# Kernel optimization log

Hardware: AMD Instinct MI355X
Metric: run time of the kernel (lower is better)

## Reference

```python
import jax, jax.numpy as jnp
import numpy as np

B_, J_, D_, E_, N_, K_ = 32, 1024, 192, 384, 16, 3


def _dwconv(x, w, b):
    # x: (B,J,E), w: (E,1,K) depthwise, b: (E,)
    xc = jnp.transpose(x, (0, 2, 1))  # (B,E,J)
    pad = w.shape[2] // 2
    y = jax.lax.conv_general_dilated(
        xc, w, window_strides=(1,), padding=[(pad, pad)],
        feature_group_count=w.shape[0], dimension_numbers=('NCH', 'OIH', 'NCH'))
    return jnp.transpose(y + b[None, :, None], (0, 2, 1))  # (B,J,E)


def _scan_dir(x, cw, cb, WB, bB, WC, bC, WD, bD, A, Wi, bi, Wr, br):
    # One directional selective-SSM pass. x: (B,J,E); A: (N,) negative diag.
    xc = _dwconv(x, cw, cb)                       # (B,J,E)
    Bt = xc @ WB + bB                             # (B,J,N)
    Ct = xc @ WC + bC                             # (B,J,N)
    Dt = jax.nn.softplus(xc @ WD + bD)            # Delta, (B,J,N)
    A_bar = jnp.exp(Dt * A)                       # ZOH discretization
    B_bar = (A_bar - 1.0) / (A + 1e-6) * Bt
    u = xc @ Wi + bi                              # in_to_state, (B,J,N)
    Bu = B_bar * u

    def step(h, ab_bu):
        ab, bu = ab_bu
        h = ab * h + bu
        return h, h

    h0 = jnp.zeros((x.shape[0], A.shape[0]), x.dtype)
    _, hs = jax.lax.scan(step, h0, (jnp.swapaxes(A_bar, 0, 1), jnp.swapaxes(Bu, 0, 1)))
    hs = jnp.swapaxes(hs, 0, 1)                   # (B,J,N)
    return (hs * Ct) @ Wr + br                    # readout, (B,J,E)


def setup_inputs() -> dict:
    key = jax.random.key(0)
    ks = iter(jax.random.split(key, 40))

    def nrm(shape, scale=0.02):
        return jax.random.normal(next(ks), shape, jnp.float32) * scale

    inp = {
        'tokens': jax.random.normal(next(ks), (B_, J_, D_), jnp.float32),
        'norm_g': jnp.ones((D_,), jnp.float32),
        'norm_b': jnp.zeros((D_,), jnp.float32),
        'Wx': nrm((D_, E_)), 'bx': jnp.zeros((E_,), jnp.float32),
        'Wz': nrm((D_, E_)), 'bz': jnp.zeros((E_,), jnp.float32),
        'convf_w': nrm((E_, 1, K_), 0.1), 'convf_b': jnp.zeros((E_,), jnp.float32),
        'convb_w': nrm((E_, 1, K_), 0.1), 'convb_b': jnp.zeros((E_,), jnp.float32),
        'WBf': nrm((E_, N_)), 'bBf': jnp.zeros((N_,), jnp.float32),
        'WCf': nrm((E_, N_)), 'bCf': jnp.zeros((N_,), jnp.float32),
        'WDf': nrm((E_, N_)), 'bDf': jnp.zeros((N_,), jnp.float32),
        'WBb': nrm((E_, N_)), 'bBb': jnp.zeros((N_,), jnp.float32),
        'WCb': nrm((E_, N_)), 'bCb': jnp.zeros((N_,), jnp.float32),
        'WDb': nrm((E_, N_)), 'bDb': jnp.zeros((N_,), jnp.float32),
        'A_log': nrm((N_,), 0.5),
        'Wi': nrm((E_, N_)), 'bi': jnp.zeros((N_,), jnp.float32),
        'Wr': nrm((N_, E_)), 'br': jnp.zeros((E_,), jnp.float32),
        'Wo': nrm((E_, D_)), 'bo': jnp.zeros((D_,), jnp.float32),
    }
    return inp


def reference(tokens, norm_g, norm_b, Wx, bx, Wz, bz, convf_w, convf_b,
              convb_w, convb_b, WBf, bBf, WCf, bCf, WDf, bDf, WBb, bBb,
              WCb, bCb, WDb, bDb, A_log, Wi, bi, Wr, br, Wo, bo):
    # LayerNorm (biased variance, eps=1e-5, like torch)
    mu = jnp.mean(tokens, axis=-1, keepdims=True)
    var = jnp.mean(jnp.square(tokens - mu), axis=-1, keepdims=True)
    t = (tokens - mu) / jnp.sqrt(var + 1e-5) * norm_g + norm_b

    x = t @ Wx + bx
    z = t @ Wz + bz
    gate = jax.nn.sigmoid(jax.nn.silu(z))

    # A computed under no_grad in torch -> stop_gradient here
    A = jax.lax.stop_gradient(-jax.nn.softplus(A_log))

    y_f = _scan_dir(x, convf_w, convf_b, WBf, bBf, WCf, bCf, WDf, bDf, A, Wi, bi, Wr, br)
    y_b = jnp.flip(_scan_dir(jnp.flip(x, 1), convb_w, convb_b, WBb, bBb, WCb, bCb,
                             WDb, bDb, A, Wi, bi, Wr, br), 1)
    y = (y_f + y_b) * gate
    return tokens + y @ Wo + bo
```

## Files before the change

### kernel.cpp

```cpp
#include <hip/hip_runtime.h>
#include <math.h>


typedef __attribute__((ext_vector_type(8))) short short8;
typedef __attribute__((ext_vector_type(4))) float f32x4;

__device__ __forceinline__ unsigned short f2bf(float f){
  union { float f; unsigned u; } v; v.f = f;
  unsigned r = v.u + 0x7FFFu + ((v.u >> 16) & 1u);
  return (unsigned short)(r >> 16);
}
__device__ __forceinline__ float bf2f(unsigned short s){
  union { unsigned u; float f; } v; v.u = ((unsigned)s) << 16;
  return v.f;
}
__device__ __forceinline__ float softplusf(float x){
  return (x > 20.f) ? x : log1pf(expf(x));
}
__device__ __forceinline__ float sigf(float x){
  return 1.f / (1.f + expf(-x));
}

__global__ __launch_bounds__(256) void prep_kernel(
    const float* __restrict__ Wx, const float* __restrict__ Wz,
    const float* __restrict__ WBf, const float* __restrict__ WCf,
    const float* __restrict__ WDf, const float* __restrict__ WBb,
    const float* __restrict__ WCb, const float* __restrict__ WDb,
    const float* __restrict__ Wi, const float* __restrict__ Wr,
    const float* __restrict__ Wo,
    const float* __restrict__ bBf, const float* __restrict__ bCf,
    const float* __restrict__ bDf, const float* __restrict__ bBb,
    const float* __restrict__ bCb, const float* __restrict__ bDb,
    const float* __restrict__ bi,
    unsigned short* __restrict__ Wxz_t, unsigned short* __restrict__ W4f_t,
    unsigned short* __restrict__ W4b_t, unsigned short* __restrict__ Wrt2,
    unsigned short* __restrict__ Wot, float* __restrict__ b4f,
    float* __restrict__ b4b)
{
  int idx = blockIdx.x * 256 + threadIdx.x;
  if (idx < 147456){ int n = idx / 192, k = idx % 192;
    Wxz_t[idx] = f2bf(n < 384 ? Wx[k*384 + n] : Wz[k*384 + n - 384]); return; }
  idx -= 147456;
  if (idx < 24576){ int n = idx / 384, k = idx % 384;
    const float* W = (n<16)?WBf:(n<32)?WCf:(n<48)?WDf:Wi;
    W4f_t[idx] = f2bf(W[k*16 + (n&15)]); return; }
  idx -= 24576;
  if (idx < 24576){ int n = idx / 384, k = idx % 384;
    const float* W = (n<16)?WBb:(n<32)?WCb:(n<48)?WDb:Wi;
    W4b_t[idx] = f2bf(W[k*16 + (n&15)]); return; }
  idx -= 24576;
  if (idx < 12288){ int n = idx / 32, k = idx % 32;
    Wrt2[idx] = f2bf(Wr[(k&15)*384 + n]); return; }
  idx -= 12288;
  if (idx < 73728){ int n = idx / 384, k = idx % 384;
    Wot[idx] = f2bf(Wo[k*192 + n]); return; }
  idx -= 73728;
  if (idx < 64){
    const float* bsel = (idx<16)?bBf:(idx<32)?bCf:(idx<48)?bDf:bi;
    b4f[idx] = bsel[idx & 15]; return; }
  idx -= 64;
  if (idx < 64){
    const float* bsel = (idx<16)?bBb:(idx<32)?bCb:(idx<48)?bDb:bi;
    b4b[idx] = bsel[idx & 15]; return; }
}

__global__ __launch_bounds__(512) void ln_xz_mfma(
    const float* __restrict__ tokens, const float* __restrict__ g,
    const float* __restrict__ nb, const unsigned short* __restrict__ Wxz_t,
    const float* __restrict__ bx, const float* __restrict__ bz,
    unsigned short* __restrict__ x_bf, unsigned short* __restrict__ gate_bf)
{
  __shared__ unsigned short t_lds[32 * 200];
  const int t = threadIdx.x;
  const int row0 = blockIdx.x * 32;

  {
    const int r = t >> 4, l16 = t & 15;
    const float* tr = tokens + (long)(row0 + r) * 192;
    float v[12], s = 0.f, sq = 0.f;
#pragma unroll
    for (int i = 0; i < 12; i++){ float x = tr[l16 + 16*i]; v[i] = x; s += x; sq += x*x; }
#pragma unroll
    for (int m = 1; m < 16; m <<= 1){ s += __shfl_xor(s, m); sq += __shfl_xor(sq, m); }
    const float mu = s * (1.f/192.f);
    const float rstd = rsqrtf(sq * (1.f/192.f) - mu*mu + 1e-5f);
#pragma unroll
    for (int i = 0; i < 12; i++){
      const int d = l16 + 16*i;
      t_lds[r*200 + d] = f2bf((v[i] - mu)*rstd*g[d] + nb[d]);
    }
  }
  __syncthreads();

  const int lane = t & 63, w = t >> 6;
  const int c0 = w * 96;
  const int l15 = lane & 15, q = lane >> 4;
  f32x4 acc[2][6];
#pragma unroll
  for (int m = 0; m < 2; m++)
#pragma unroll
    for (int n = 0; n < 6; n++) acc[m][n] = (f32x4){0.f,0.f,0.f,0.f};

  const unsigned short* wb = Wxz_t + (long)(c0 + l15)*192 + q*8;
#pragma unroll
  for (int ks = 0; ks < 6; ks++){
    const int k0 = ks * 32;
    short8 a0 = *(const short8*)&t_lds[l15*200 + k0 + q*8];
    short8 a1 = *(const short8*)&t_lds[(16 + l15)*200 + k0 + q*8];
#pragma unroll
    for (int nf = 0; nf < 6; nf++){
      short8 bw = *(const short8*)&wb[nf*16*192 + k0];
      acc[0][nf] = __builtin_amdgcn_mfma_f32_16x16x32_bf16(a0, bw, acc[0][nf], 0, 0, 0);
      acc[1][nf] = __builtin_amdgcn_mfma_f32_16x16x32_bf16(a1, bw, acc[1][nf], 0, 0, 0);
    }
  }
#pragma unroll
  for (int nf = 0; nf < 6; nf++){
    const int c = c0 + nf*16 + l15;
    if (c < 384){
      const float bv = bx[c];
#pragma unroll
      for (int m = 0; m < 2; m++)
#pragma unroll
        for (int r = 0; r < 4; r++){
          const long R = row0 + m*16 + q*4 + r;
          x_bf[R*384 + c] = f2bf(acc[m][nf][r] + bv);
        }
    } else {
      const int cz = c - 384;
      const float bv = bz[cz];
#pragma unroll
      for (int m = 0; m < 2; m++)
#pragma unroll
        for (int r = 0; r < 4; r++){
          const long R = row0 + m*16 + q*4 + r;
          const float z = acc[m][nf][r] + bv;
          gate_bf[R*384 + cz] = f2bf(sigf(z * sigf(z)));
        }
    }
  }
}

__global__ __launch_bounds__(256) void proj_mfma(
    const unsigned short* __restrict__ x_bf,
    const float* __restrict__ cwf, const float* __restrict__ cbf,
    const float* __restrict__ cwb, const float* __restrict__ cbb,
    const unsigned short* __restrict__ W4f, const unsigned short* __restrict__ W4b,
    const float* __restrict__ b4f, const float* __restrict__ b4b,
    const float* __restrict__ A_log,
    float* __restrict__ Af, float* __restrict__ Buf, float* __restrict__ Ctf,
    float* __restrict__ Ab, float* __restrict__ Bub, float* __restrict__ Ctb)
{
  __shared__ unsigned short xc[64 * 392];
  float* trans = (float*)xc;
  const int t = threadIdx.x;
  const int dir = blockIdx.x >> 9;
  const int bid = blockIdx.x & 511;
  const int b  = bid >> 4;
  const int j0 = (bid & 15) * 64;
  const float* cw = dir ? cwb : cwf;
  const float* cb = dir ? cbb : cbf;
  const unsigned short* W4 = dir ? W4b : W4f;
  const float* b4 = dir ? b4b : b4f;
  float* Aout = dir ? Ab  : Af;
  float* Bout = dir ? Bub : Buf;
  float* Cout = dir ? Ctb : Ctf;

  {
    const long xrow = (long)b * 1024 * 384;
#pragma unroll
    for (int i = 0; i < 12; i++){
      const int idx = i*256 + t;
      const int r = idx / 48;
      const int e0 = (idx - r*48) * 8;
      const int jp = j0 + r;
      short8 xm = (short8){0,0,0,0,0,0,0,0};
      short8 xp = (short8){0,0,0,0,0,0,0,0};
      if (jp >= 1){
        const int js = dir ? 1024 - jp : jp - 1;
        xm = *(const short8*)&x_bf[xrow + (long)js*384 + e0];
      }
      short8 x0;
      {
        const int js = dir ? 1023 - jp : jp;
        x0 = *(const short8*)&x_bf[xrow + (long)js*384 + e0];
      }
      if (jp <= 1022){
        const int js = dir ? 1022 - jp : jp + 1;
        xp = *(const short8*)&x_bf[xrow + (long)js*384 + e0];
      }
      float wv[24], cbv[8];
#pragma unroll
      for (int v = 0; v < 6; v++)
        *(float4*)&wv[v*4] = *(const float4*)&cw[e0*3 + v*4];
#pragma unroll
      for (int v = 0; v < 2; v++)
        *(float4*)&cbv[v*4] = *(const float4*)&cb[e0 + v*4];
      short8 o;
#pragma unroll
      for (int m = 0; m < 8; m++){
        const float acc = fmaf(wv[3*m],   bf2f((unsigned short)xm[m]),
                          fmaf(wv[3*m+1], bf2f((unsigned short)x0[m]),
                          fmaf(wv[3*m+2], bf2f((unsigned short)xp[m]), cbv[m])));
        o[m] = (short)f2bf(acc);
      }
      *(short8*)&xc[r*392 + e0] = o;
    }
  }
  __syncthreads();

  const int lane = t & 63, w = t >> 6;
  const int l15 = lane & 15, q = lane >> 4;
  f32x4 acc[4];
#pragma unroll
  for (int nf = 0; nf < 4; nf++) acc[nf] = (f32x4){0.f,0.f,0.f,0.f};
  const unsigned short* wb = W4 + (long)l15*384 + q*8;
#pragma unroll
  for (int ks = 0; ks < 12; ks++){
    const int k0 = ks * 32;
    short8 a = *(const short8*)&xc[(w*16 + l15)*392 + k0 + q*8];
#pragma unroll
    for (int nf = 0; nf < 4; nf++){
      short8 bw = *(const short8*)&wb[nf*16*384 + k0];
      acc[nf] = __builtin_amdgcn_mfma_f32_16x16x32_bf16(a, bw, acc[nf], 0, 0, 0);
    }
  }
  __syncthreads();

  {
    const int n = l15;
    const float Av = -softplusf(A_log[n]);
    const float bB = b4[n], bC = b4[16+n], bD = b4[32+n], bU = b4[48+n];
#pragma unroll
    for (int r = 0; r < 4; r++){
      const int row = w*16 + q*4 + r;
      const float Bt  = acc[0][r] + bB;
      const float Ctv = acc[1][r] + bC;
      const float dt  = softplusf(acc[2][r] + bD);
      const float u   = acc[3][r] + bU;
      const float ab  = expf(dt * Av);
      const float bu  = (ab - 1.f) / (Av + 1e-6f) * Bt * u;
      trans[(0*16 + n)*66 + row] = ab;
      trans[(1*16 + n)*66 + row] = bu;
      trans[(2*16 + n)*66 + row] = Ctv;
    }
  }
  __syncthreads();

  {
    const int j = t & 63, n4 = t >> 6;
#pragma unroll
    for (int i = 0; i < 4; i++){
      const int n = n4*4 + i;
      const int jp = j0 + j;
      const long base = ((long)b*16 + n) * 1024;
      Aout[base + jp] = trans[(0*16 + n)*66 + j];
      Bout[base + jp] = trans[(1*16 + n)*66 + j];
      Cout[base + (dir ? 1023 - jp : jp)] = trans[(2*16 + n)*66 + j];
    }
  }
}

__global__ __launch_bounds__(256) void scan2_kernel(
    const float* __restrict__ Af, const float* __restrict__ Buf, float* __restrict__ hsf,
    const float* __restrict__ Ab, const float* __restrict__ Bub, float* __restrict__ hsb)
{
  __shared__ float sA[256], sB[256];
  const int sel = blockIdx.x >> 9;
  const long base = (long)(blockIdx.x & 511) * 1024;
  const float* Abar = sel ? Ab  : Af;
  const float* Bu   = sel ? Bub : Buf;
  float* hs         = sel ? hsb : hsf;
  const int t = threadIdx.x;
  const float4 a4 = *reinterpret_cast<const float4*>(&Abar[base + t*4]);
  const float4 b4 = *reinterpret_cast<const float4*>(&Bu[base + t*4]);
  float A = a4.x, Bc = b4.x;
  Bc = fmaf(a4.y, Bc, b4.y); A *= a4.y;
  Bc = fmaf(a4.z, Bc, b4.z); A *= a4.z;
  Bc = fmaf(a4.w, Bc, b4.w); A *= a4.w;
  sA[t] = A; sB[t] = Bc;
  __syncthreads();
  for (int off = 1; off < 256; off <<= 1){
    const float cA = sA[t], cB = sB[t];
    float pA = 1.f, pB = 0.f;
    if (t >= off){ pA = sA[t - off]; pB = sB[t - off]; }
    __syncthreads();
    sA[t] = pA * cA;
    sB[t] = fmaf(cA, pB, cB);
    __syncthreads();
  }
  float h = (t > 0) ? sB[t - 1] : 0.f;
  float4 o;
  h = fmaf(a4.x, h, b4.x); o.x = h;
  h = fmaf(a4.y, h, b4.y); o.y = h;
  h = fmaf(a4.z, h, b4.z); o.z = h;
  h = fmaf(a4.w, h, b4.w); o.w = h;
  *reinterpret_cast<float4*>(&hs[base + t*4]) = o;
}

__global__ __launch_bounds__(256) void final_mfma(
    const float* __restrict__ tokens, const unsigned short* __restrict__ gate_bf,
    const float* __restrict__ hsf, const float* __restrict__ Ctf,
    const float* __restrict__ hsb, const float* __restrict__ Ctb,
    const unsigned short* __restrict__ Wrt2, const float* __restrict__ br,
    const unsigned short* __restrict__ Wot, const float* __restrict__ bo,
    float* __restrict__ out)
{
  __shared__ unsigned short s2[64 * 40];
  __shared__ unsigned short yg[64 * 392];
  const int t = threadIdx.x;
  const int b  = blockIdx.x >> 4;
  const int j0 = (blockIdx.x & 15) * 64;

  {
    const int j = t & 63, grp = t >> 6;
#pragma unroll
    for (int i = 0; i < 8; i++){
      const int kk = grp*8 + i;
      float val;
      if (kk < 16){
        const long p = ((long)b*16 + kk)*1024 + j0 + j;
        val = hsf[p] * Ctf[p];
      } else {
        const long basen = ((long)b*16 + (kk - 16)) * 1024;
        val = hsb[basen + 1023 - (j0 + j)] * Ctb[basen + j0 + j];
      }
      s2[j*40 + kk] = f2bf(val);
    }
  }
  __syncthreads();

  const int lane = t & 63, w = t >> 6;
  const int l15 = lane & 15, q = lane >> 4;

  {
    short8 a = *(const short8*)&s2[(w*16 + l15)*40 + q*8];
    const unsigned short* wbp = Wrt2 + (long)l15*32 + q*8;
#pragma unroll
    for (int nf = 0; nf < 24; nf++){
      short8 bw = *(const short8*)&wbp[nf*16*32];
      f32x4 acc = (f32x4){0.f,0.f,0.f,0.f};
      acc = __builtin_amdgcn_mfma_f32_16x16x32_bf16(a, bw, acc, 0, 0, 0);
      const int c = nf*16 + l15;
      const float brv = 2.f * br[c];
#pragma unroll
      for (int r = 0; r < 4; r++){
        const int row = w*16 + q*4 + r;
        const long R = (long)b*1024 + j0 + row;
        const float gv = bf2f(gate_bf[R*384 + c]);
        yg[row*392 + c] = f2bf((acc[r] + brv) * gv);
      }
    }
  }
  __syncthreads();

  {
    f32x4 acc[12];
#pragma unroll
    for (int nf = 0; nf < 12; nf++) acc[nf] = (f32x4){0.f,0.f,0.f,0.f};
    const unsigned short* wbp = Wot + (long)l15*384 + q*8;
#pragma unroll
    for (int ks = 0; ks < 12; ks++){
      const int k0 = ks * 32;
      short8 a = *(const short8*)&yg[(w*16 + l15)*392 + k0 + q*8];
#pragma unroll
      for (int nf = 0; nf < 12; nf++){
        short8 bw = *(const short8*)&wbp[(long)nf*16*384 + k0];
        acc[nf] = __builtin_amdgcn_mfma_f32_16x16x32_bf16(a, bw, acc[nf], 0, 0, 0);
      }
    }
#pragma unroll
    for (int nf = 0; nf < 12; nf++){
      const int c = nf*16 + l15;
      const float bv = bo[c];
#pragma unroll
      for (int r = 0; r < 4; r++){
        const int row = w*16 + q*4 + r;
        const long R = (long)b*1024 + j0 + row;
        out[R*192 + c] = tokens[R*192 + c] + acc[nf][r] + bv;
      }
    }
  }
}

extern "C" void kernel_launch(void* const* d_in, const int* in_sizes, int n_in,
                              void* d_out, int out_size, void* d_ws, size_t ws_size,
                              hipStream_t stream)
{
  const float* tokens  = (const float*)d_in[0];
  const float* norm_g  = (const float*)d_in[1];
  const float* norm_b  = (const float*)d_in[2];
  const float* Wx      = (const float*)d_in[3];
  const float* bx      = (const float*)d_in[4];
  const float* Wz      = (const float*)d_in[5];
  const float* bz      = (const float*)d_in[6];
  const float* convf_w = (const float*)d_in[7];
  const float* convf_b = (const float*)d_in[8];
  const float* convb_w = (const float*)d_in[9];
  const float* convb_b = (const float*)d_in[10];
  const float* WBf     = (const float*)d_in[11];
  const float* bBf     = (const float*)d_in[12];
  const float* WCf     = (const float*)d_in[13];
  const float* bCf     = (const float*)d_in[14];
  const float* WDf     = (const float*)d_in[15];
  const float* bDf     = (const float*)d_in[16];
  const float* WBb     = (const float*)d_in[17];
  const float* bBb     = (const float*)d_in[18];
  const float* WCb     = (const float*)d_in[19];
  const float* bCb     = (const float*)d_in[20];
  const float* WDb     = (const float*)d_in[21];
  const float* bDb     = (const float*)d_in[22];
  const float* A_log   = (const float*)d_in[23];
  const float* Wi      = (const float*)d_in[24];
  const float* bi      = (const float*)d_in[25];
  const float* Wr      = (const float*)d_in[26];
  const float* br      = (const float*)d_in[27];
  const float* Wo      = (const float*)d_in[28];
  const float* bo      = (const float*)d_in[29];

  char* ws = (char*)d_ws;
  unsigned short* x_bf    = (unsigned short*)(ws + 0);
  unsigned short* gate_bf = (unsigned short*)(ws + 25165824);
  unsigned short* Wxz_t   = (unsigned short*)(ws + 50331648);
  unsigned short* W4f_t   = (unsigned short*)(ws + 50626560);
  unsigned short* W4b_t   = (unsigned short*)(ws + 50675712);
  unsigned short* Wrt2    = (unsigned short*)(ws + 50724864);
  unsigned short* Wot     = (unsigned short*)(ws + 50749440);
  float* b4f = (float*)(ws + 50896896);
  float* b4b = (float*)(ws + 50897152);
  float* Af  = (float*)(ws + 50897408);
  float* Buf = (float*)(ws + 52994560);
  float* Ctf = (float*)(ws + 55091712);
  float* hsf = (float*)(ws + 57188864);
  float* Ab  = (float*)(ws + 59286016);
  float* Bub = (float*)(ws + 61383168);
  float* Ctb = (float*)(ws + 63480320);
  float* hsb = (float*)(ws + 65577472);

  prep_kernel<<<1105, 256, 0, stream>>>(Wx, Wz, WBf, WCf, WDf, WBb, WCb, WDb,
                                        Wi, Wr, Wo, bBf, bCf, bDf, bBb, bCb, bDb, bi,
                                        Wxz_t, W4f_t, W4b_t, Wrt2, Wot, b4f, b4b);
  ln_xz_mfma<<<1024, 512, 0, stream>>>(tokens, norm_g, norm_b, Wxz_t, bx, bz,
                                       x_bf, gate_bf);
  proj_mfma<<<1024, 256, 0, stream>>>(x_bf, convf_w, convf_b, convb_w, convb_b,
                                      W4f_t, W4b_t, b4f, b4b, A_log,
                                      Af, Buf, Ctf, Ab, Bub, Ctb);
  scan2_kernel<<<1024, 256, 0, stream>>>(Af, Buf, hsf, Ab, Bub, hsb);
  final_mfma<<<512, 256, 0, stream>>>(tokens, gate_bf, hsf, Ctf, hsb, Ctb,
                                      Wrt2, br, Wot, bo, (float*)d_out);
}
```

Before: 159.4 us.

## Stage MFMA outputs through LDS for coalesced vector stores and gate loads

In the LN/x-z projection kernel, MFMA results are now written to a swizzled LDS tile and stored to global memory as 16-byte vectors rather than scattered 2-byte stores. The sigmoid uses a fast exp and a hardware reciprocal. In the final readout kernel, the gate multiply becomes a separate vectorized pass over LDS, and the output projection is staged through LDS so the residual add and output store use float4 accesses. This trades extra LDS space, more barriers and slightly lower sigmoid precision for fewer uncoalesced global transactions.

```diff
diff --git a/kernel.cpp b/kernel.cpp
--- a/kernel.cpp
+++ b/kernel.cpp
@@ -17,8 +17,8 @@
 __device__ __forceinline__ float softplusf(float x){
   return (x > 20.f) ? x : log1pf(expf(x));
 }
-__device__ __forceinline__ float sigf(float x){
-  return 1.f / (1.f + expf(-x));
+__device__ __forceinline__ float sigf_fast(float x){
+  return __builtin_amdgcn_rcpf(1.f + __expf(-x));
 }
 
 __global__ __launch_bounds__(256) void prep_kernel(
@@ -71,6 +71,7 @@
     unsigned short* __restrict__ x_bf, unsigned short* __restrict__ gate_bf)
 {
   __shared__ unsigned short t_lds[32 * 200];
+  __shared__ unsigned short out_lds[32 * 784];
   const int t = threadIdx.x;
   const int row0 = blockIdx.x * 32;
 
@@ -114,29 +115,50 @@
       acc[1][nf] = __builtin_amdgcn_mfma_f32_16x16x32_bf16(a1, bw, acc[1][nf], 0, 0, 0);
     }
   }
+
 #pragma unroll
   for (int nf = 0; nf < 6; nf++){
     const int c = c0 + nf*16 + l15;
+    const int scol = c0 + ((nf + q) % 6)*16 + l15;
     if (c < 384){
       const float bv = bx[c];
 #pragma unroll
       for (int m = 0; m < 2; m++)
 #pragma unroll
         for (int r = 0; r < 4; r++){
-          const long R = row0 + m*16 + q*4 + r;
-          x_bf[R*384 + c] = f2bf(acc[m][nf][r] + bv);
+          const int row = m*16 + q*4 + r;
+          out_lds[row*784 + scol] = f2bf(acc[m][nf][r] + bv);
         }
     } else {
-      const int cz = c - 384;
-      const float bv = bz[cz];
+      const float bv = bz[c - 384];
 #pragma unroll
       for (int m = 0; m < 2; m++)
 #pragma unroll
         for (int r = 0; r < 4; r++){
-          const long R = row0 + m*16 + q*4 + r;
+          const int row = m*16 + q*4 + r;
           const float z = acc[m][nf][r] + bv;
-          gate_bf[R*384 + cz] = f2bf(sigf(z * sigf(z)));
+          const float si = z * sigf_fast(z);
+          out_lds[row*784 + scol] = f2bf(sigf_fast(si));
         }
+    }
+  }
+  __syncthreads();
+
+  {
+#pragma unroll
+    for (int i = 0; i < 6; i++){
+      const int item = i*512 + t;
+      const int row  = item / 96;
+      const int cblk = item % 96;
+      const int c_out = cblk * 8;
+      const int qq = (row >> 2) & 3;
+      const int ws = c_out / 96;
+      const int nfl = (c_out % 96) / 16;
+      const int scol = ws*96 + ((nfl + qq) % 6)*16 + (c_out % 16);
+      short8 v = *(const short8*)&out_lds[row*784 + scol];
+      const long R = (long)row0 + row;
+      if (c_out < 384) *(short8*)&x_bf[R*384 + c_out] = v;
+      else             *(short8*)&gate_bf[R*384 + (c_out - 384)] = v;
     }
   }
 }
@@ -346,16 +368,31 @@
 #pragma unroll
       for (int r = 0; r < 4; r++){
         const int row = w*16 + q*4 + r;
-        const long R = (long)b*1024 + j0 + row;
-        const float gv = bf2f(gate_bf[R*384 + c]);
-        yg[row*392 + c] = f2bf((acc[r] + brv) * gv);
-      }
-    }
-  }
-  __syncthreads();
-
-  {
-    f32x4 acc[12];
+        yg[row*392 + c] = f2bf(acc[r] + brv);
+      }
+    }
+  }
+  __syncthreads();
+
+  {
+#pragma unroll
+    for (int i = 0; i < 12; i++){
+      const int item = i*256 + t;
+      const int row = item / 48;
+      const int cb  = (item % 48) * 8;
+      short8 y8 = *(const short8*)&yg[row*392 + cb];
+      short8 g8 = *(const short8*)&gate_bf[((long)b*1024 + j0 + row)*384 + cb];
+      short8 o;
+#pragma unroll
+      for (int m = 0; m < 8; m++)
+        o[m] = (short)f2bf(bf2f((unsigned short)y8[m]) * bf2f((unsigned short)g8[m]));
+      *(short8*)&yg[row*392 + cb] = o;
+    }
+  }
+  __syncthreads();
+
+  f32x4 acc[12];
+  {
 #pragma unroll
     for (int nf = 0; nf < 12; nf++) acc[nf] = (f32x4){0.f,0.f,0.f,0.f};
     const unsigned short* wbp = Wot + (long)l15*384 + q*8;
@@ -369,16 +406,41 @@
         acc[nf] = __builtin_amdgcn_mfma_f32_16x16x32_bf16(a, bw, acc[nf], 0, 0, 0);
       }
     }
+  }
+  __syncthreads();
+
+  float* stg = (float*)yg;
+  {
+    const int gq = q ^ (q >> 1);
 #pragma unroll
     for (int nf = 0; nf < 12; nf++){
       const int c = nf*16 + l15;
       const float bv = bo[c];
+      const int scol = ((nf + gq) % 12)*16 + l15;
 #pragma unroll
       for (int r = 0; r < 4; r++){
         const int row = w*16 + q*4 + r;
-        const long R = (long)b*1024 + j0 + row;
-        out[R*192 + c] = tokens[R*192 + c] + acc[nf][r] + bv;
-      }
+        stg[row*196 + scol] = acc[nf][r] + bv;
+      }
+    }
+  }
+  __syncthreads();
+
+  {
+#pragma unroll
+    for (int i = 0; i < 12; i++){
+      const int item = i*256 + t;
+      const int row = item / 48;
+      const int c4  = (item % 48) * 4;
+      const int qq = (row >> 2) & 3;
+      const int gg = qq ^ (qq >> 1);
+      const int nf = c4 / 16;
+      const int scol = ((nf + gg) % 12)*16 + (c4 % 16);
+      float4 v = *(const float4*)&stg[row*196 + scol];
+      const long R = (long)b*1024 + j0 + row;
+      const float4 tk = *(const float4*)&tokens[R*192 + c4];
+      v.x += tk.x; v.y += tk.y; v.z += tk.z; v.w += tk.w;
+      *(float4*)&out[R*192 + c4] = v;
     }
   }
 }
```

Result: faster. 152.3 us (-4.5%).
